# Performance work log

Measured on AMD Instinct MI355X. Metric: run time of the kernel, lower is better.

The kernel has to match this reference:

```python
import jax, jax.numpy as jnp
import numpy as np

B, T, D, H = 16384, 48, 32, 64  # batch, num_lags, input_dim(num_features), hidden_size


def setup_inputs() -> dict:
    key = jax.random.key(0)
    ks = jax.random.split(key, 8)
    s = 1.0 / np.sqrt(H)  # torch-style uniform bound magnitude, approximated via scaled normal
    return {
        "x": jax.random.normal(ks[0], (B, T, D), dtype=jnp.float32),
        "h0": jax.random.normal(ks[1], (B, H), dtype=jnp.float32) * 0.01,
        "c0": jax.random.normal(ks[2], (B, H), dtype=jnp.float32) * 0.01,
        "W_att": jax.random.normal(ks[3], (1, 2 * H + T), dtype=jnp.float32) * 0.05,
        "b_att": jnp.zeros((1,), dtype=jnp.float32),
        "W_ih": jax.random.normal(ks[4], (4 * H, D), dtype=jnp.float32) * s,
        "W_hh": jax.random.normal(ks[5], (4 * H, H), dtype=jnp.float32) * s,
        "b_ih": jnp.zeros((4 * H,), dtype=jnp.float32),
        "b_hh": jnp.zeros((4 * H,), dtype=jnp.float32),
    }


def reference(x, h0, c0, W_att, b_att, W_ih, W_hh, b_ih, b_hh):
    # x: [B, T, D];  input-attention DA-RNN encoder with single-layer LSTM.
    Bn, Tn, Dn = x.shape
    Hn = h0.shape[-1]
    xT = jnp.transpose(x, (0, 2, 1))  # [B, D, T] full per-feature series, constant over t
    w_att = W_att[0]                   # [2H+T]

    def step(carry, xt):
        ht, ct = carry  # [B, H]
        hrep = jnp.broadcast_to(ht[:, None, :], (Bn, Dn, Hn))
        crep = jnp.broadcast_to(ct[:, None, :], (Bn, Dn, Hn))
        feat = jnp.concatenate([hrep, crep, xT], axis=2)  # [B, D, 2H+T]
        et = jnp.einsum('bdf,f->bd', feat, w_att) + b_att[0]  # [B, D]
        at = jax.nn.softmax(et, axis=1)                        # softmax over features
        wi = at * xt                                           # [B, D]
        gates = wi @ W_ih.T + b_ih + ht @ W_hh.T + b_hh        # [B, 4H]
        i_g, f_g, g_g, o_g = jnp.split(gates, 4, axis=1)
        i_g = jax.nn.sigmoid(i_g)
        f_g = jax.nn.sigmoid(f_g)
        g_g = jnp.tanh(g_g)
        o_g = jax.nn.sigmoid(o_g)
        ct2 = f_g * ct + i_g * g_g
        ht2 = o_g * jnp.tanh(ct2)
        return (ht2, ct2), (at, ht2)

    xs = jnp.transpose(x, (1, 0, 2))  # [T, B, D]
    _, (ats, hts) = jax.lax.scan(step, (h0, c0), xs)
    attention = jnp.transpose(ats, (1, 0, 2))       # [B, T, D]
    input_encoded = jnp.transpose(hts, (1, 0, 2))   # [B, T, H]
    return attention, input_encoded
```

## Files before the change

kernel.cpp:

```cpp
#include <hip/hip_runtime.h>

#define TT 48
#define DD 32
#define HH 64
#define BB 16384
#define LOG2E 1.4426950408889634f

typedef __bf16 bf16x8 __attribute__((ext_vector_type(8)));
typedef float f32x4 __attribute__((ext_vector_type(4)));

#define MFMA(a, b, c) __builtin_amdgcn_mfma_f32_16x16x32_bf16(a, b, c, 0, 0, 0)
#define BC(v) __builtin_bit_cast(bf16x8, v)

static __device__ __forceinline__ float exp2_f(float v) {
#if __has_builtin(__builtin_amdgcn_exp2f)
  return __builtin_amdgcn_exp2f(v);
#else
  return exp2f(v);
#endif
}
static __device__ __forceinline__ unsigned short bfu(float f) {
  __bf16 b = (__bf16)f;
  return __builtin_bit_cast(unsigned short, b);
}
static __device__ __forceinline__ float sigm2(float y) {
  return __builtin_amdgcn_rcpf(1.f + exp2_f(-y));
}
static __device__ __forceinline__ float tanh2(float y) {
  return fmaf(-2.f, __builtin_amdgcn_rcpf(1.f + exp2_f(y)), 1.f);
}


__global__ void prep_kernel(const float* __restrict__ W_ih, const float* __restrict__ W_hh,
                            const float* __restrict__ b_ih, const float* __restrict__ b_hh,
                            unsigned short* __restrict__ WhhL, unsigned short* __restrict__ WihL,
                            float* __restrict__ bsumL) {
  const int tid = threadIdx.x;
  const int l = tid & 63, qt = tid >> 6;
  const int rowl = l & 15, kq = (l >> 4) * 8;
  for (int mm = 0; mm < 4; ++mm) {
    const int m = qt * 4 + mm;
    const int g = m >> 2, hq = m & 3;
    const float s = (g == 2) ? 2.f * LOG2E : LOG2E;
    const int hidx = (hq >> 1) * 32 + (rowl >> 2) * 8 + (hq & 1) * 4 + (rowl & 3);
    const int orig = g * 64 + hidx;
    for (int c = 0; c < 2; ++c)
      for (int j = 0; j < 8; ++j)
        WhhL[(m * 2 + c) * 512 + l * 8 + j] = bfu(W_hh[orig * 64 + c * 32 + kq + j] * s);
    for (int j = 0; j < 8; ++j)
      WihL[m * 512 + l * 8 + j] = bfu(W_ih[orig * 32 + kq + j] * s);
    if ((l >> 4) == 0) bsumL[m * 16 + rowl] = (b_ih[orig] + b_hh[orig]) * s;
  }
}

__global__ __launch_bounds__(256, 1) void lstm_kernel(
    const float* __restrict__ x, const float* __restrict__ h0, const float* __restrict__ c0,
    const float* __restrict__ W_att, const unsigned short* __restrict__ WhhL,
    const unsigned short* __restrict__ WihL, const float* __restrict__ bsumL,
    float* __restrict__ out0, float* __restrict__ out1) {
  const int tid = threadIdx.x;
  const int l = tid & 63;
  const int wid = tid >> 6;
  const int b = l & 15;
  const int qp = l >> 4;
  const int brow = blockIdx.x * 64 + wid * 16 + b;

  f32x4 whhHi[16][2], wihR[16], biasR[16];
#pragma unroll
  for (int m = 0; m < 16; ++m) {
#pragma unroll
    for (int c = 0; c < 2; ++c)
      whhHi[m][c] = *(const f32x4*)(WhhL + ((m * 2 + c) << 9) + l * 8);
    wihR[m] = *(const f32x4*)(WihL + (m << 9) + l * 8);
    biasR[m] = *(const f32x4*)(bsumL + m * 16 + qp * 4);
  }
#pragma unroll
  for (int m = 0; m < 16; ++m) {
#pragma unroll
    for (int c = 0; c < 2; ++c) asm volatile("" : "+v"(whhHi[m][c]));
    asm volatile("" : "+a"(wihR[m]));
    asm volatile("" : "+a"(biasR[m]));
  }

  const float* xp = x + (size_t)brow * (TT * DD) + qp * 8;

  float p[8];
#pragma unroll
  for (int j = 0; j < 8; ++j) p[j] = 0.f;
#pragma unroll 4
  for (int t = 0; t < TT; ++t) {
    const float w = W_att[2 * HH + t];
    float4 x0 = *(const float4*)(xp + t * DD);
    float4 x1 = *(const float4*)(xp + t * DD + 4);
    p[0] = fmaf(x0.x, w, p[0]); p[1] = fmaf(x0.y, w, p[1]);
    p[2] = fmaf(x0.z, w, p[2]); p[3] = fmaf(x0.w, w, p[3]);
    p[4] = fmaf(x1.x, w, p[4]); p[5] = fmaf(x1.y, w, p[5]);
    p[6] = fmaf(x1.z, w, p[6]); p[7] = fmaf(x1.w, w, p[7]);
  }
  float av[8];
  {
    float mx = fmaxf(fmaxf(fmaxf(p[0], p[1]), fmaxf(p[2], p[3])),
                     fmaxf(fmaxf(p[4], p[5]), fmaxf(p[6], p[7])));
    mx = fmaxf(mx, __shfl_xor(mx, 16));
    mx = fmaxf(mx, __shfl_xor(mx, 32));
    float s = 0.f;
#pragma unroll
    for (int j = 0; j < 8; ++j) {
      av[j] = exp2_f((p[j] - mx) * LOG2E);
      s += av[j];
    }
    s += __shfl_xor(s, 16);
    s += __shfl_xor(s, 32);
    float inv = __builtin_amdgcn_rcpf(s);
#pragma unroll
    for (int j = 0; j < 8; ++j) av[j] *= inv;
  }
  float4 av0, av1;
  av0.x = av[0]; av0.y = av[1]; av0.z = av[2]; av0.w = av[3];
  av1.x = av[4]; av1.y = av[5]; av1.z = av[6]; av1.w = av[7];
  float* o0 = out0 + (size_t)brow * (TT * DD) + qp * 8;

  f32x4 creg[4];
#pragma unroll
  for (int hq = 0; hq < 4; ++hq)
    creg[hq] = *(const f32x4*)(c0 + (size_t)brow * HH + (hq >> 1) * 32 + qp * 8 + (hq & 1) * 4);

  bf16x8 bh[2];
#pragma unroll
  for (int c = 0; c < 2; ++c) {
    const float* hp = h0 + (size_t)brow * HH + c * 32 + qp * 8;
    float4 v0 = *(const float4*)hp, v1 = *(const float4*)(hp + 4);
    float vv[8] = {v0.x, v0.y, v0.z, v0.w, v1.x, v1.y, v1.z, v1.w};
#pragma unroll
    for (int j = 0; j < 8; ++j) bh[c][j] = (__bf16)vv[j];
  }

  float* op = out1 + (size_t)brow * (TT * HH);
  float xv[8];
  {
    float4 x0 = *(const float4*)xp, x1 = *(const float4*)(xp + 4);
    xv[0] = x0.x; xv[1] = x0.y; xv[2] = x0.z; xv[3] = x0.w;
    xv[4] = x1.x; xv[5] = x1.y; xv[6] = x1.z; xv[7] = x1.w;
  }

#pragma unroll 1
  for (int t = 0; t < TT; ++t) {
    *(float4*)(o0 + t * DD) = av0;
    *(float4*)(o0 + t * DD + 4) = av1;
    bf16x8 bxw;
#pragma unroll
    for (int j = 0; j < 8; ++j) bxw[j] = (__bf16)(xv[j] * av[j]);
    const int tn = (t + 1 < TT) ? (t + 1) : (TT - 1);
    float xn[8];
    {
      const float* xnp = xp + (size_t)tn * DD;
      float4 x0 = *(const float4*)xnp, x1 = *(const float4*)(xnp + 4);
      xn[0] = x0.x; xn[1] = x0.y; xn[2] = x0.z; xn[3] = x0.w;
      xn[4] = x1.x; xn[5] = x1.y; xn[6] = x1.z; xn[7] = x1.w;
    }

    bf16x8 nbh[2];
#pragma unroll
    for (int hq = 0; hq < 4; ++hq) {
      f32x4 acc[4];
#pragma unroll
      for (int g = 0; g < 4; ++g) {
        const int m = g * 4 + hq;
        f32x4 A = MFMA(BC(whhHi[m][0]), bh[0], biasR[m]);
        A = MFMA(BC(whhHi[m][1]), bh[1], A);
        A = MFMA(BC(wihR[m]), bxw, A);
        acc[g] = A;
      }
      float hr[4];
#pragma unroll
      for (int r = 0; r < 4; ++r) {
        float ig = sigm2(acc[0][r]);
        float fg = sigm2(acc[1][r]);
        float gt = tanh2(acc[2][r]);
        float og = sigm2(acc[3][r]);
        float cn = fg * creg[hq][r] + ig * gt;
        creg[hq][r] = cn;
        hr[r] = og * tanh2(2.f * LOG2E * cn);
      }
      float4 hv;
      hv.x = hr[0]; hv.y = hr[1]; hv.z = hr[2]; hv.w = hr[3];
      *(float4*)(op + (size_t)t * HH + (hq >> 1) * 32 + qp * 8 + (hq & 1) * 4) = hv;
#pragma unroll
      for (int r = 0; r < 4; ++r) nbh[hq >> 1][(hq & 1) * 4 + r] = (__bf16)hr[r];
    }
    bh[0] = nbh[0];
    bh[1] = nbh[1];
#pragma unroll
    for (int j = 0; j < 8; ++j) xv[j] = xn[j];
  }
}

extern "C" void kernel_launch(void* const* d_in, const int* in_sizes, int n_in,
                              void* d_out, int out_size, void* d_ws, size_t ws_size,
                              hipStream_t stream) {
  const float* x = (const float*)d_in[0];
  const float* h0 = (const float*)d_in[1];
  const float* c0 = (const float*)d_in[2];
  const float* W_att = (const float*)d_in[3];
  const float* W_ih = (const float*)d_in[5];
  const float* W_hh = (const float*)d_in[6];
  const float* b_ih = (const float*)d_in[7];
  const float* b_hh = (const float*)d_in[8];

  float* out0 = (float*)d_out;
  float* out1 = out0 + (size_t)BB * TT * DD;

  char* ws = (char*)d_ws;
  unsigned short* WhhL = (unsigned short*)ws;
  unsigned short* WihL = (unsigned short*)(ws + 32768);
  float* bsumL = (float*)(ws + 49152);

  prep_kernel<<<1, 256, 0, stream>>>(W_ih, W_hh, b_ih, b_hh, WhhL, WihL, bsumL);
  lstm_kernel<<<BB / 64, 256, 0, stream>>>(x, h0, c0, W_att, WhhL, WihL, bsumL, out0, out1);
}
```

Measured before the change: 121.0 us.

## Split each batch tile's hidden units across two waves with LDS h exchange

Each 16-row batch tile is now handled by two waves, each owning half of the hidden units. They exchange bf16 hidden state through double-buffered shared memory and a barrier every timestep. This halves per-wave weight registers and serial MFMA/activation work per step, giving four times as many blocks for more parallelism across the recurrence. The attention output is now written once before the loop by one wave, and the cell state is kept pre-scaled to save a multiply. The cost is a per-step LDS round trip and block barrier.

```diff
diff --git a/kernel.cpp b/kernel.cpp
--- a/kernel.cpp
+++ b/kernel.cpp
@@ -53,52 +53,59 @@
   }
 }
 
-__global__ __launch_bounds__(256, 1) void lstm_kernel(
+__global__ __launch_bounds__(128, 2) void lstm_kernel(
     const float* __restrict__ x, const float* __restrict__ h0, const float* __restrict__ c0,
     const float* __restrict__ W_att, const unsigned short* __restrict__ WhhL,
     const unsigned short* __restrict__ WihL, const float* __restrict__ bsumL,
     float* __restrict__ out0, float* __restrict__ out1) {
+  __shared__ __align__(16) char xch[4096];
   const int tid = threadIdx.x;
   const int l = tid & 63;
-  const int wid = tid >> 6;
+  const int half = tid >> 6;
   const int b = l & 15;
   const int qp = l >> 4;
-  const int brow = blockIdx.x * 64 + wid * 16 + b;
-
-  f32x4 whhHi[16][2], wihR[16], biasR[16];
-#pragma unroll
-  for (int m = 0; m < 16; ++m) {
-#pragma unroll
-    for (int c = 0; c < 2; ++c)
-      whhHi[m][c] = *(const f32x4*)(WhhL + ((m * 2 + c) << 9) + l * 8);
-    wihR[m] = *(const f32x4*)(WihL + (m << 9) + l * 8);
-    biasR[m] = *(const f32x4*)(bsumL + m * 16 + qp * 4);
-  }
-#pragma unroll
-  for (int m = 0; m < 16; ++m) {
-#pragma unroll
-    for (int c = 0; c < 2; ++c) asm volatile("" : "+v"(whhHi[m][c]));
-    asm volatile("" : "+a"(wihR[m]));
-    asm volatile("" : "+a"(biasR[m]));
-  }
+  const int brow = blockIdx.x * 16 + b;
+
+#define XOFF(buf, hf) (((buf) * 2 + (hf)) * 1024)
+
+  f32x4 whhO[2][4], whhX[2][4], wihR[2][4], biasR[2][4];
+#pragma unroll
+  for (int e = 0; e < 2; ++e)
+#pragma unroll
+    for (int g = 0; g < 4; ++g) {
+      const int m = g * 4 + 2 * half + e;
+      whhO[e][g] = *(const f32x4*)(WhhL + ((m * 2 + half) << 9) + l * 8);
+      whhX[e][g] = *(const f32x4*)(WhhL + ((m * 2 + (1 ^ half)) << 9) + l * 8);
+      wihR[e][g] = *(const f32x4*)(WihL + (m << 9) + l * 8);
+      biasR[e][g] = *(const f32x4*)(bsumL + m * 16 + qp * 4);
+    }
+#pragma unroll
+  for (int e = 0; e < 2; ++e)
+#pragma unroll
+    for (int g = 0; g < 4; ++g) {
+      asm volatile("" : "+v"(whhO[e][g]));
+      asm volatile("" : "+v"(whhX[e][g]));
+      asm volatile("" : "+a"(wihR[e][g]));
+      asm volatile("" : "+a"(biasR[e][g]));
+    }
 
   const float* xp = x + (size_t)brow * (TT * DD) + qp * 8;
 
-  float p[8];
-#pragma unroll
-  for (int j = 0; j < 8; ++j) p[j] = 0.f;
-#pragma unroll 4
-  for (int t = 0; t < TT; ++t) {
-    const float w = W_att[2 * HH + t];
-    float4 x0 = *(const float4*)(xp + t * DD);
-    float4 x1 = *(const float4*)(xp + t * DD + 4);
-    p[0] = fmaf(x0.x, w, p[0]); p[1] = fmaf(x0.y, w, p[1]);
-    p[2] = fmaf(x0.z, w, p[2]); p[3] = fmaf(x0.w, w, p[3]);
-    p[4] = fmaf(x1.x, w, p[4]); p[5] = fmaf(x1.y, w, p[5]);
-    p[6] = fmaf(x1.z, w, p[6]); p[7] = fmaf(x1.w, w, p[7]);
-  }
   float av[8];
   {
+    float p[8];
+#pragma unroll
+    for (int j = 0; j < 8; ++j) p[j] = 0.f;
+#pragma unroll 4
+    for (int t = 0; t < TT; ++t) {
+      const float w = W_att[2 * HH + t];
+      float4 x0 = *(const float4*)(xp + t * DD);
+      float4 x1 = *(const float4*)(xp + t * DD + 4);
+      p[0] = fmaf(x0.x, w, p[0]); p[1] = fmaf(x0.y, w, p[1]);
+      p[2] = fmaf(x0.z, w, p[2]); p[3] = fmaf(x0.w, w, p[3]);
+      p[4] = fmaf(x1.x, w, p[4]); p[5] = fmaf(x1.y, w, p[5]);
+      p[6] = fmaf(x1.z, w, p[6]); p[7] = fmaf(x1.w, w, p[7]);
+    }
     float mx = fmaxf(fmaxf(fmaxf(p[0], p[1]), fmaxf(p[2], p[3])),
                      fmaxf(fmaxf(p[4], p[5]), fmaxf(p[6], p[7])));
     mx = fmaxf(mx, __shfl_xor(mx, 16));
@@ -114,61 +121,71 @@
     float inv = __builtin_amdgcn_rcpf(s);
 #pragma unroll
     for (int j = 0; j < 8; ++j) av[j] *= inv;
-  }
-  float4 av0, av1;
-  av0.x = av[0]; av0.y = av[1]; av0.z = av[2]; av0.w = av[3];
-  av1.x = av[4]; av1.y = av[5]; av1.z = av[6]; av1.w = av[7];
-  float* o0 = out0 + (size_t)brow * (TT * DD) + qp * 8;
-
-  f32x4 creg[4];
-#pragma unroll
-  for (int hq = 0; hq < 4; ++hq)
-    creg[hq] = *(const f32x4*)(c0 + (size_t)brow * HH + (hq >> 1) * 32 + qp * 8 + (hq & 1) * 4);
-
-  bf16x8 bh[2];
-#pragma unroll
-  for (int c = 0; c < 2; ++c) {
-    const float* hp = h0 + (size_t)brow * HH + c * 32 + qp * 8;
+    if (half == 0) {
+      float4 a0, a1;
+      a0.x = av[0]; a0.y = av[1]; a0.z = av[2]; a0.w = av[3];
+      a1.x = av[4]; a1.y = av[5]; a1.z = av[6]; a1.w = av[7];
+      float* o0 = out0 + (size_t)brow * (TT * DD) + qp * 8;
+#pragma unroll 4
+      for (int t = 0; t < TT; ++t) {
+        *(float4*)(o0 + t * DD) = a0;
+        *(float4*)(o0 + t * DD + 4) = a1;
+      }
+    }
+  }
+
+  f32x4 creg[2];
+#pragma unroll
+  for (int e = 0; e < 2; ++e) {
+    f32x4 cv = *(const f32x4*)(c0 + (size_t)brow * HH + half * 32 + qp * 8 + e * 4);
+#pragma unroll
+    for (int r = 0; r < 4; ++r) cv[r] *= 2.f * LOG2E;
+    creg[e] = cv;
+  }
+
+  bf16x8 own;
+  {
+    const float* hp = h0 + (size_t)brow * HH + half * 32 + qp * 8;
     float4 v0 = *(const float4*)hp, v1 = *(const float4*)(hp + 4);
     float vv[8] = {v0.x, v0.y, v0.z, v0.w, v1.x, v1.y, v1.z, v1.w};
 #pragma unroll
-    for (int j = 0; j < 8; ++j) bh[c][j] = (__bf16)vv[j];
-  }
-
-  float* op = out1 + (size_t)brow * (TT * HH);
+    for (int j = 0; j < 8; ++j) own[j] = (__bf16)vv[j];
+    *(f32x4*)(xch + XOFF(0, half) + l * 16) = __builtin_bit_cast(f32x4, own);
+  }
+
+  float* op = out1 + (size_t)brow * (TT * HH) + half * 32 + qp * 8;
   float xv[8];
   {
     float4 x0 = *(const float4*)xp, x1 = *(const float4*)(xp + 4);
     xv[0] = x0.x; xv[1] = x0.y; xv[2] = x0.z; xv[3] = x0.w;
     xv[4] = x1.x; xv[5] = x1.y; xv[6] = x1.z; xv[7] = x1.w;
   }
+  __syncthreads();
 
 #pragma unroll 1
   for (int t = 0; t < TT; ++t) {
-    *(float4*)(o0 + t * DD) = av0;
-    *(float4*)(o0 + t * DD + 4) = av1;
+    const int cur = t & 1, nxt = cur ^ 1;
+    bf16x8 oth = BC(*(const f32x4*)(xch + XOFF(cur, 1 ^ half) + l * 16));
     bf16x8 bxw;
 #pragma unroll
     for (int j = 0; j < 8; ++j) bxw[j] = (__bf16)(xv[j] * av[j]);
     const int tn = (t + 1 < TT) ? (t + 1) : (TT - 1);
-    float xn[8];
     {
       const float* xnp = xp + (size_t)tn * DD;
       float4 x0 = *(const float4*)xnp, x1 = *(const float4*)(xnp + 4);
-      xn[0] = x0.x; xn[1] = x0.y; xn[2] = x0.z; xn[3] = x0.w;
-      xn[4] = x1.x; xn[5] = x1.y; xn[6] = x1.z; xn[7] = x1.w;
-    }
-
-    bf16x8 nbh[2];
-#pragma unroll
-    for (int hq = 0; hq < 4; ++hq) {
+      xv[0] = x0.x; xv[1] = x0.y; xv[2] = x0.z; xv[3] = x0.w;
+      xv[4] = x1.x; xv[5] = x1.y; xv[6] = x1.z; xv[7] = x1.w;
+    }
+
+    bf16x8 ownNew;
+#pragma unroll
+    for (int e = 0; e < 2; ++e) {
       f32x4 acc[4];
 #pragma unroll
       for (int g = 0; g < 4; ++g) {
-        const int m = g * 4 + hq;
-        f32x4 A = MFMA(BC(whhHi[m][0]), bh[0], biasR[m]);
-        A = MFMA(BC(whhHi[m][1]), bh[1], A);
-        A = MFMA(BC(wihR[m]), bxw, A);
+        f32x4 A = MFMA(BC(wihR[e][g]), bxw, biasR[e][g]);
+        A = MFMA(BC(whhO[e][g]), own, A);
+        A = MFMA(BC(whhX[e][g]), oth, A);
         acc[g] = A;
       }
       float hr[4];
@@ -176,23 +193,27 @@
       for (int r = 0; r < 4; ++r) {
         float ig = sigm2(acc[0][r]);
         float fg = sigm2(acc[1][r]);
-        float gt = tanh2(acc[2][r]);
+        float gts = fmaf(-4.f * LOG2E,
+                         __builtin_amdgcn_rcpf(1.f + exp2_f(acc[2][r])), 2.f * LOG2E);
         float og = sigm2(acc[3][r]);
-        float cn = fg * creg[hq][r] + ig * gt;
-        creg[hq][r] = cn;
-        hr[r] = og * tanh2(2.f * LOG2E * cn);
+        float cns = fmaf(fg, creg[e][r], ig * gts);
+        creg[e][r] = cns;
+        hr[r] = og * tanh2(cns);
       }
       float4 hv;
       hv.x = hr[0]; hv.y = hr[1]; hv.z = hr[2]; hv.w = hr[3];
-      *(float4*)(op + (size_t)t * HH + (hq >> 1) * 32 + qp * 8 + (hq & 1) * 4) = hv;
-#pragma unroll
-      for (int r = 0; r < 4; ++r) nbh[hq >> 1][(hq & 1) * 4 + r] = (__bf16)hr[r];
-    }
-    bh[0] = nbh[0];
-    bh[1] = nbh[1];
-#pragma unroll
-    for (int j = 0; j < 8; ++j) xv[j] = xn[j];
-  }
+      *(float4*)(op + (size_t)t * HH + e * 4) = hv;
+#pragma unroll
+      for (int r = 0; r < 4; ++r) ownNew[e * 4 + r] = (__bf16)hr[r];
+    }
+    own = ownNew;
+    *(f32x4*)(xch + XOFF(nxt, half) + l * 16) = __builtin_bit_cast(f32x4, own);
+    asm volatile("s_waitcnt lgkmcnt(0)" ::: "memory");
+    __builtin_amdgcn_sched_barrier(0);
+    __builtin_amdgcn_s_barrier();
+    __builtin_amdgcn_sched_barrier(0);
+  }
+#undef XOFF
 }
 
 extern "C" void kernel_launch(void* const* d_in, const int* in_sizes, int n_in,
@@ -216,5 +237,5 @@
   float* bsumL = (float*)(ws + 49152);
 
   prep_kernel<<<1, 256, 0, stream>>>(W_ih, W_hh, b_ih, b_hh, WhhL, WihL, bsumL);
-  lstm_kernel<<<BB / 64, 256, 0, stream>>>(x, h0, c0, W_att, WhhL, WihL, bsumL, out0, out1);
-}
+  lstm_kernel<<<BB / 16, 128, 0, stream>>>(x, h0, c0, W_att, WhhL, WihL, bsumL, out0, out1);
+}
```

After: 183.1 us. 1.51x slower.
